# Performance work log

Hardware: AMD Instinct MI355X
Metric: run time of the kernel (lower is better)

The kernel has to match this reference:

```python
import jax, jax.numpy as jnp
from jax import lax
import numpy as np

TAG_NAMES = ["O", "B-MAT", "I-MAT", "B-PRO", "I-PRO", "B-APL", "I-APL", "B-SMT", "I-SMT", "B-CMT", "I-CMT", "B-DSC", "I-DSC"]
IMP = -100.0


def _init_crf_params(key):
    # torchcrf initializes uniform(-0.1, 0.1); CRF_NEW then clamps invalid
    # BIO transitions to -100 per define_invalid_crf_transitions/init_crf_transitions.
    K = len(TAG_NAMES)
    k1, k2, k3 = jax.random.split(key, 3)
    start = np.array(jax.random.uniform(k1, (K,), minval=-0.1, maxval=0.1), dtype=np.float32)
    end = np.array(jax.random.uniform(k2, (K,), minval=-0.1, maxval=0.1), dtype=np.float32)
    trans = np.array(jax.random.uniform(k3, (K, K), minval=-0.1, maxval=0.1), dtype=np.float32)
    pref = [t[0] for t in TAG_NAMES]
    ent = [t.split('-')[1] if '-' in t else '' for t in TAG_NAMES]
    for i in range(K):
        if pref[i] in ('B', 'I'):  # invalid begin/end for BIO
            start[i] = IMP
            end[i] = IMP
    for i in range(K):
        for j in range(K):
            # invalid_transitions_position: O -> I  (B->P, I->P are empty sets)
            if pref[i] == 'O' and pref[j] == 'I':
                trans[i, j] = IMP
            # invalid_transitions_tags: B->I, I->I across different entity types
            if pref[i] in ('B', 'I') and pref[j] == 'I' and ent[i] != ent[j]:
                trans[i, j] = IMP
    return jnp.asarray(start), jnp.asarray(end), jnp.asarray(trans)


def setup_inputs() -> dict:
    key = jax.random.key(0)
    k_em, k_tag, k_p = jax.random.split(key, 3)
    B, T, K = 4096, 512, len(TAG_NAMES)
    emissions = jax.random.normal(k_em, (B, T, K), dtype=jnp.float32)
    tags = jax.random.randint(k_tag, (B, T), 0, K, dtype=jnp.int64)
    mask = jnp.ones((B, T), dtype=bool)
    start_transitions, end_transitions, transitions = _init_crf_params(k_p)
    return {"emissions": emissions, "tags": tags, "mask": mask,
            "start_transitions": start_transitions,
            "end_transitions": end_transitions,
            "transitions": transitions}


def reference(emissions, tags, mask, start_transitions, end_transitions, transitions):
    # torchcrf CRF.forward with batch_first=True, reduction='sum':
    # returns sum over batch of log p(tags | emissions).
    B, T, K = emissions.shape
    maskf = mask.astype(emissions.dtype)

    # ---- numerator: score of the given tag path ----
    emit = jnp.take_along_axis(emissions, tags[..., None], axis=2)[..., 0]  # [B,T]
    trans = transitions[tags[:, :-1], tags[:, 1:]]                           # [B,T-1]
    num = start_transitions[tags[:, 0]] + emit[:, 0]
    num = num + jnp.sum((trans + emit[:, 1:]) * maskf[:, 1:], axis=1)
    seq_ends = jnp.sum(mask.astype(jnp.int32), axis=1) - 1                   # [B]
    last_tags = tags[jnp.arange(B), seq_ends]
    num = num + end_transitions[last_tags]

    # ---- denominator: log partition via forward-algorithm scan over time ----
    em_t = jnp.swapaxes(emissions, 0, 1)   # [T,B,K]
    mask_t = jnp.swapaxes(mask, 0, 1)      # [T,B]
    score0 = start_transitions + em_t[0]   # [B,K]

    def step(score, xs):
        em, m = xs  # em: [B,K], m: [B]
        # broadcast: [B,K_from,1] + [K_from,K_to] + [B,1,K_to]
        nxt = jax.nn.logsumexp(score[:, :, None] + transitions[None] + em[:, None, :], axis=1)
        return jnp.where(m[:, None], nxt, score), None

    score, _ = lax.scan(step, score0, (em_t[1:], mask_t[1:]))
    denom = jax.nn.logsumexp(score + end_transitions, axis=1)  # [B]

    return jnp.sum(num - denom)
```

## Files before the change

### kernel.cpp

```cpp
#include <hip/hip_runtime.h>


typedef float  f4  __attribute__((ext_vector_type(4)));
typedef float  f4u __attribute__((ext_vector_type(4), aligned(4)));
typedef int    i2  __attribute__((ext_vector_type(2)));
typedef int    i4  __attribute__((ext_vector_type(4)));
typedef __bf16 bh8 __attribute__((ext_vector_type(8)));

#define FENCE do { __builtin_amdgcn_sched_barrier(0); \
                   asm volatile("" ::: "memory"); } while (0)

__device__ __forceinline__ unsigned pack_bf16(float x, float y) {
  return __builtin_amdgcn_perm(__float_as_uint(y) + 0x8000u,
                               __float_as_uint(x) + 0x8000u, 0x07060302u);
}

__global__ void __launch_bounds__(128, 1)
crf_main(const float* __restrict__ em,
         const int*   __restrict__ tags,
         const float* __restrict__ startT,
         const float* __restrict__ endT,
         const float* __restrict__ trans,
         float* __restrict__ partial)
{
  __shared__ float ldsT[256];
  __shared__ float ldsS[16], ldsE[16];
  __shared__ float pFa[256];
  __shared__ float lsF[16], numF[16], resB[16];
  __shared__ int   tag255[16];

  const int tid = threadIdx.x;
  for (int i = tid; i < 169; i += 128) {
    const int r_ = i / 13, c_ = i - r_ * 13;
    ldsT[r_ * 16 + c_] = trans[i];
  }
  if (tid < 13) ldsS[tid] = startT[tid];
  if (tid >= 16 && tid < 29) ldsE[tid - 16] = endT[tid - 16];
  __syncthreads();

  const int lane = tid & 63;
  const int n    = lane & 15;
  const int q    = lane >> 4;
  const bool is_fwd = (tid < 64);
  const int seq  = blockIdx.x * 16 + n;
  const int loadBase = (q < 3) ? 4 * q : 9;
  const int lo       = (q < 3) ? 4 * q : 12;
  const unsigned span = (q < 3) ? 3u : 0u;
  const float* emP = em + (size_t)seq * 6656 + loadBase;
  const int*   tgP = tags + (size_t)seq * 512;

  bh8 afrag;
  {
    float av[4];
#pragma unroll
    for (int i = 0; i < 4; ++i) {
      const int kk = 4 * q + i;
      av[i] = (kk < 13 && n < 13)
            ? __expf(is_fwd ? ldsT[kk * 16 + n] : ldsT[n * 16 + kk]) : 0.0f;
    }
    i4 ai = { (int)pack_bf16(av[0], av[1]), (int)pack_bf16(av[2], av[3]), 0, 0 };
    afrag = __builtin_bit_cast(bh8, ai);
  }

  f4 D;
#pragma unroll
  for (int r = 0; r < 4; ++r) {
    const int m = 4 * q + r;
    D[r] = (m < 13) ? __expf(is_fwd ? ldsS[m] : ldsE[m]) : 0.0f;
  }

  int   ls2 = 0;
  int   epend = 0;
  float rcCur = 1.0f;
  float em_acc = 0.0f, trans_acc = 0.0f;
  float sDs0 = 0, sDs1 = 0, sDs2 = 0, sDs3 = 0;
  float start_t0 = 0.0f;
  int tg_hi = 0, tg_lo = 0, tg511 = 0;
  f4 eA[16], eB[16];
  int4 tA[4], tB[4];

#define TGV(TB, k) ((((k) & 3) == 0) ? TB[(k) >> 2].x : (((k) & 3) == 1) ? TB[(k) >> 2].y \
                  : (((k) & 3) == 2) ? TB[(k) >> 2].z : TB[(k) >> 2].w)

#define LOADC(EB, TB, TC) do {                                          \
    const int tc_ = (TC);                                               \
    _Pragma("unroll")                                                   \
    for (int k_ = 0; k_ < 16; ++k_)                                     \
      EB[k_] = *(const f4u*)(emP + (size_t)(tc_ + k_) * 13);            \
    _Pragma("unroll")                                                   \
    for (int g_ = 0; g_ < 4; ++g_)                                      \
      TB[g_] = *(const int4*)(tgP + tc_ + 4 * g_);                      \
  } while (0)

#define RNMEAS() do {                                                   \
    float cm_ = fmaxf(fmaxf(Ds0, Ds1), fmaxf(Ds2, Ds3));                \
    cm_ = fmaxf(cm_, __shfl_xor(cm_, 16, 64));                          \
    cm_ = fmaxf(cm_, __shfl_xor(cm_, 32, 64));                          \
    const int eb_ = (int)(__float_as_uint(cm_) >> 23);                  \
    epend = eb_ - 126;                                                  \
    rcCur = __uint_as_float((unsigned)(253 - eb_) << 23);               \
  } while (0)

#define CORE(EM4, KPH, TGVv) do {                                       \
    float e0 = __expf((q == 3) ? (EM4).w : (EM4).x);                    \
    float e1 = __expf((EM4).y);                                         \
    float e2 = __expf((EM4).z);                                         \
    float e3 = __expf((EM4).w);                                         \
    if ((KPH) == 7) { e0 *= rcCur; e1 *= rcCur; e2 *= rcCur; e3 *= rcCur; \
                      ls2 += epend; }                                   \
    Ds0 = D[0] * e0; Ds1 = D[1] * e1; Ds2 = D[2] * e2; Ds3 = D[3] * e3; \
    if ((KPH) == 5) RNMEAS();                                           \
    {                                                                   \
      const unsigned ur_ = (unsigned)((TGVv) - lo);                     \
      const int rr_ = (TGVv) - loadBase;                                \
      const float s01_ = (rr_ & 1) ? (EM4).y : (EM4).x;                 \
      const float s23_ = (rr_ & 1) ? (EM4).w : (EM4).z;                 \
      const float sv_  = (rr_ & 2) ? s23_ : s01_;                       \
      em_acc += (ur_ <= span) ? sv_ : 0.0f;                             \
    }                                                                   \
    {                                                                   \
      i4 bi_ = { (int)pack_bf16(Ds0, Ds1), (int)pack_bf16(Ds2, Ds3), 0, 0 }; \
      bh8 bf_ = __builtin_bit_cast(bh8, bi_);                           \
      D = __builtin_amdgcn_mfma_f32_16x16x32_bf16(                      \
              afrag, bf_, (f4){0.f, 0.f, 0.f, 0.f}, 0, 0, 0);           \
    }                                                                   \
  } while (0)

#define PROCF(EB, TB, FIRST, LAST) do {                                 \
    _Pragma("unroll")                                                   \
    for (int k = 0; k < 16; ++k) {                                      \
      const int tgv = TGV(TB, k);                                       \
      if (FIRST && k == 0) start_t0 = ldsS[tgv];                        \
      else {                                                            \
        const int pv = (k == 0) ? tg_hi : TGV(TB, k - 1);               \
        trans_acc += ldsT[pv * 16 + tgv];                               \
      }                                                                 \
      const f4 em4 = EB[k];                                             \
      float Ds0, Ds1, Ds2, Ds3;                                         \
      CORE(em4, (k & 7), tgv);                                          \
      if (LAST && k == 15) { sDs0 = Ds0; sDs1 = Ds1; sDs2 = Ds2; sDs3 = Ds3; } \
    }                                                                   \
    tg_hi = TGV(TB, 15);                                                \
  } while (0)

#define PROCB(EB, TB, FIRST) do {                                       \
    if (FIRST) tg511 = TGV(TB, 15);                                     \
    else       trans_acc += ldsT[TGV(TB, 15) * 16 + tg_lo];             \
    _Pragma("unroll")                                                   \
    for (int kk = 0; kk < 16; ++kk) {                                   \
      const int k = 15 - kk;                                            \
      const int tgv = TGV(TB, k);                                       \
      if (k > 0) trans_acc += ldsT[TGV(TB, k - 1) * 16 + tgv];          \
      const f4 em4 = EB[k];                                             \
      float Ds0, Ds1, Ds2, Ds3;                                         \
      CORE(em4, (kk & 7), tgv);                                         \
    }                                                                   \
    tg_lo = TGV(TB, 0);                                                 \
  } while (0)

  if (is_fwd) {
    LOADC(eA, tA, 0); LOADC(eB, tB, 16); FENCE;
    PROCF(eA, tA, true, false);
    for (int it = 0; it < 7; ++it) {
      LOADC(eA, tA, 32 * it + 32); FENCE;
      PROCF(eB, tB, false, false);
      LOADC(eB, tB, 32 * it + 48); FENCE;
      PROCF(eA, tA, false, false);
    }
    FENCE;
    PROCF(eB, tB, false, true);
    float emr = em_acc + __shfl_xor(em_acc, 16, 64);
    emr += __shfl_xor(emr, 32, 64);
    if (q == 0) {
      lsF[n]    = (float)ls2 * 0.6931471805599453f;
      numF[n]   = start_t0 + emr + trans_acc;
      tag255[n] = tg_hi;
    }
    *(f4*)&pFa[n * 16 + 4 * q] = (f4){sDs0, sDs1, sDs2, sDs3};
  } else {
    LOADC(eA, tA, 496); LOADC(eB, tB, 480); FENCE;
    PROCB(eA, tA, true);
    for (int it = 0; it < 7; ++it) {
      LOADC(eA, tA, 464 - 32 * it); FENCE;
      PROCB(eB, tB, false);
      LOADC(eB, tB, 448 - 32 * it); FENCE;
      PROCB(eA, tA, false);
    }
    FENCE;
    PROCB(eB, tB, false);
  }

  __syncthreads();

  if (!is_fwd) {
    const f4 al = *(const f4*)&pFa[n * 16 + 4 * q];
    float z = al[0] * D[0] + al[1] * D[1] + al[2] * D[2] + al[3] * D[3];
    z += __shfl_xor(z, 16, 64);
    z += __shfl_xor(z, 32, 64);
    float emr = em_acc + __shfl_xor(em_acc, 16, 64);
    emr += __shfl_xor(emr, 32, 64);
    const float denom = lsF[n] + (float)ls2 * 0.6931471805599453f + __logf(z);
    const float num   = numF[n] + emr + trans_acc
                      + ldsT[tag255[n] * 16 + tg_lo]
                      + ldsE[tg511];
    if (q == 0) resB[n] = num - denom;
  }
  __syncthreads();
  if (tid == 0) {
    float s = 0.0f;
#pragma unroll
    for (int i = 0; i < 16; ++i) s += resB[i];
    partial[blockIdx.x] = s;
  }

#undef TGV
#undef LOADC
#undef RNMEAS
#undef CORE
#undef PROCF
#undef PROCB
}

__global__ void __launch_bounds__(256)
crf_reduce(const float* __restrict__ part, float* __restrict__ out, int n)
{
  float v = 0.0f;
  for (int i = threadIdx.x; i < n; i += 256) v += part[i];
#pragma unroll
  for (int off = 32; off > 0; off >>= 1) v += __shfl_down(v, off);
  __shared__ float w[4];
  if ((threadIdx.x & 63) == 0) w[threadIdx.x >> 6] = v;
  __syncthreads();
  if (threadIdx.x == 0) out[0] = (w[0] + w[1]) + (w[2] + w[3]);
}

extern "C" void kernel_launch(void* const* d_in, const int* in_sizes, int n_in,
                              void* d_out, int out_size, void* d_ws, size_t ws_size,
                              hipStream_t stream) {
  const float* em   = (const float*)d_in[0];
  const int*   tags = (const int*)d_in[1];
  const float* st   = (const float*)d_in[3];
  const float* en   = (const float*)d_in[4];
  const float* tr   = (const float*)d_in[5];
  float* part = (float*)d_ws;

  crf_main<<<256, 128, 0, stream>>>(em, tags, st, en, tr, part);
  crf_reduce<<<1, 256, 0, stream>>>(part, (float*)d_out, 256);
}
```

Measured before the change: 186.8 us.

## Offload CRF numerator scoring to a dedicated third wavefront per block

Adds a third wave per block that computes the gold-path numerator (emission gather plus start, transition and end scores), splitting each sequence into four time chunks across lane groups. The forward and backward recurrence waves no longer load tags or accumulate numerator terms, which shortens their serial MFMA critical path. In exchange the new wave issues scattered scalar emission gathers that compete for memory bandwidth, and the block grows to 192 threads.

```diff
diff --git a/kernel.cpp b/kernel.cpp
--- a/kernel.cpp
+++ b/kernel.cpp
@@ -3,7 +3,6 @@
 
 typedef float  f4  __attribute__((ext_vector_type(4)));
 typedef float  f4u __attribute__((ext_vector_type(4), aligned(4)));
-typedef int    i2  __attribute__((ext_vector_type(2)));
 typedef int    i4  __attribute__((ext_vector_type(4)));
 typedef __bf16 bh8 __attribute__((ext_vector_type(8)));
 
@@ -15,7 +14,7 @@
                                __float_as_uint(x) + 0x8000u, 0x07060302u);
 }
 
-__global__ void __launch_bounds__(128, 1)
+__global__ void __launch_bounds__(192, 1)
 crf_main(const float* __restrict__ em,
          const int*   __restrict__ tags,
          const float* __restrict__ startT,
@@ -27,10 +26,9 @@
   __shared__ float ldsS[16], ldsE[16];
   __shared__ float pFa[256];
   __shared__ float lsF[16], numF[16], resB[16];
-  __shared__ int   tag255[16];
 
   const int tid = threadIdx.x;
-  for (int i = tid; i < 169; i += 128) {
+  for (int i = tid; i < 169; i += 192) {
     const int r_ = i / 13, c_ = i - r_ * 13;
     ldsT[r_ * 16 + c_] = trans[i];
   }
@@ -39,57 +37,74 @@
   __syncthreads();
 
   const int lane = tid & 63;
+  const int wv   = tid >> 6;
   const int n    = lane & 15;
   const int q    = lane >> 4;
-  const bool is_fwd = (tid < 64);
-  const int seq  = blockIdx.x * 16 + n;
-  const int loadBase = (q < 3) ? 4 * q : 9;
-  const int lo       = (q < 3) ? 4 * q : 12;
-  const unsigned span = (q < 3) ? 3u : 0u;
-  const float* emP = em + (size_t)seq * 6656 + loadBase;
-  const int*   tgP = tags + (size_t)seq * 512;
-
-  bh8 afrag;
-  {
-    float av[4];
-#pragma unroll
-    for (int i = 0; i < 4; ++i) {
-      const int kk = 4 * q + i;
-      av[i] = (kk < 13 && n < 13)
-            ? __expf(is_fwd ? ldsT[kk * 16 + n] : ldsT[n * 16 + kk]) : 0.0f;
-    }
-    i4 ai = { (int)pack_bf16(av[0], av[1]), (int)pack_bf16(av[2], av[3]), 0, 0 };
-    afrag = __builtin_bit_cast(bh8, ai);
-  }
-
-  f4 D;
-#pragma unroll
-  for (int r = 0; r < 4; ++r) {
-    const int m = 4 * q + r;
-    D[r] = (m < 13) ? __expf(is_fwd ? ldsS[m] : ldsE[m]) : 0.0f;
-  }
-
-  int   ls2 = 0;
-  int   epend = 0;
-  float rcCur = 1.0f;
-  float em_acc = 0.0f, trans_acc = 0.0f;
+
+  f4  D = {0.f, 0.f, 0.f, 0.f};
+  int ls2 = 0;
   float sDs0 = 0, sDs1 = 0, sDs2 = 0, sDs3 = 0;
-  float start_t0 = 0.0f;
-  int tg_hi = 0, tg_lo = 0, tg511 = 0;
-  f4 eA[16], eB[16];
-  int4 tA[4], tB[4];
-
-#define TGV(TB, k) ((((k) & 3) == 0) ? TB[(k) >> 2].x : (((k) & 3) == 1) ? TB[(k) >> 2].y \
-                  : (((k) & 3) == 2) ? TB[(k) >> 2].z : TB[(k) >> 2].w)
-
-#define LOADC(EB, TB, TC) do {                                          \
+
+  if (wv == 2) {
+    const int s = q;
+    const int seq = blockIdx.x * 16 + n;
+    const int* tq = tags + (size_t)seq * 512;
+    const float* emQ = em + (size_t)seq * 6656;
+    const int t0base = 128 * s;
+    float nacc = 0.0f;
+    int prev = (s > 0) ? tq[t0base - 1] : 0;
+#pragma unroll 4
+    for (int g = 0; g < 32; ++g) {
+      const int t0 = t0base + 4 * g;
+      const int4 tv = *(const int4*)(tq + t0);
+      nacc += emQ[(size_t)(t0 + 0) * 13 + tv.x];
+      nacc += emQ[(size_t)(t0 + 1) * 13 + tv.y];
+      nacc += emQ[(size_t)(t0 + 2) * 13 + tv.z];
+      nacc += emQ[(size_t)(t0 + 3) * 13 + tv.w];
+      if (!(s == 0 && g == 0)) nacc += ldsT[prev * 16 + tv.x];
+      nacc += ldsT[tv.x * 16 + tv.y] + ldsT[tv.y * 16 + tv.z]
+            + ldsT[tv.z * 16 + tv.w];
+      prev = tv.w;
+    }
+    if (s == 0) nacc += ldsS[tq[0]];
+    if (s == 3) nacc += ldsE[prev];
+    nacc += __shfl_xor(nacc, 16, 64);
+    nacc += __shfl_xor(nacc, 32, 64);
+    if (s == 0) numF[n] = nacc;
+  } else {
+    const bool is_fwd = (wv == 0);
+    const int seq = blockIdx.x * 16 + n;
+    const int loadBase = (q < 3) ? 4 * q : 9;
+    const float* emP = em + (size_t)seq * 6656 + loadBase;
+
+    bh8 afrag;
+    {
+      float av[4];
+#pragma unroll
+      for (int i = 0; i < 4; ++i) {
+        const int kk = 4 * q + i;
+        av[i] = (kk < 13 && n < 13)
+              ? __expf(is_fwd ? ldsT[kk * 16 + n] : ldsT[n * 16 + kk]) : 0.0f;
+      }
+      i4 ai = { (int)pack_bf16(av[0], av[1]), (int)pack_bf16(av[2], av[3]), 0, 0 };
+      afrag = __builtin_bit_cast(bh8, ai);
+    }
+
+#pragma unroll
+    for (int r = 0; r < 4; ++r) {
+      const int m = 4 * q + r;
+      D[r] = (m < 13) ? __expf(is_fwd ? ldsS[m] : ldsE[m]) : 0.0f;
+    }
+
+    int   epend = 0;
+    float rcCur = 1.0f;
+    f4 eA[16], eB[16];
+
+#define LOADE(EB, TC) do {                                              \
     const int tc_ = (TC);                                               \
     _Pragma("unroll")                                                   \
     for (int k_ = 0; k_ < 16; ++k_)                                     \
       EB[k_] = *(const f4u*)(emP + (size_t)(tc_ + k_) * 13);            \
-    _Pragma("unroll")                                                   \
-    for (int g_ = 0; g_ < 4; ++g_)                                      \
-      TB[g_] = *(const int4*)(tgP + tc_ + 4 * g_);                      \
   } while (0)
 
 #define RNMEAS() do {                                                   \
@@ -101,7 +116,7 @@
     rcCur = __uint_as_float((unsigned)(253 - eb_) << 23);               \
   } while (0)
 
-#define CORE(EM4, KPH, TGVv) do {                                       \
+#define CORE(EM4, KPH) do {                                             \
     float e0 = __expf((q == 3) ? (EM4).w : (EM4).x);                    \
     float e1 = __expf((EM4).y);                                         \
     float e2 = __expf((EM4).z);                                         \
@@ -111,14 +126,6 @@
     Ds0 = D[0] * e0; Ds1 = D[1] * e1; Ds2 = D[2] * e2; Ds3 = D[3] * e3; \
     if ((KPH) == 5) RNMEAS();                                           \
     {                                                                   \
-      const unsigned ur_ = (unsigned)((TGVv) - lo);                     \
-      const int rr_ = (TGVv) - loadBase;                                \
-      const float s01_ = (rr_ & 1) ? (EM4).y : (EM4).x;                 \
-      const float s23_ = (rr_ & 1) ? (EM4).w : (EM4).z;                 \
-      const float sv_  = (rr_ & 2) ? s23_ : s01_;                       \
-      em_acc += (ur_ <= span) ? sv_ : 0.0f;                             \
-    }                                                                   \
-    {                                                                   \
       i4 bi_ = { (int)pack_bf16(Ds0, Ds1), (int)pack_bf16(Ds2, Ds3), 0, 0 }; \
       bh8 bf_ = __builtin_bit_cast(bh8, bi_);                           \
       D = __builtin_amdgcn_mfma_f32_16x16x32_bf16(                      \
@@ -126,84 +133,66 @@
     }                                                                   \
   } while (0)
 
-#define PROCF(EB, TB, FIRST, LAST) do {                                 \
+#define PROCF(EB, LAST) do {                                            \
     _Pragma("unroll")                                                   \
     for (int k = 0; k < 16; ++k) {                                      \
-      const int tgv = TGV(TB, k);                                       \
-      if (FIRST && k == 0) start_t0 = ldsS[tgv];                        \
-      else {                                                            \
-        const int pv = (k == 0) ? tg_hi : TGV(TB, k - 1);               \
-        trans_acc += ldsT[pv * 16 + tgv];                               \
-      }                                                                 \
       const f4 em4 = EB[k];                                             \
       float Ds0, Ds1, Ds2, Ds3;                                         \
-      CORE(em4, (k & 7), tgv);                                          \
-      if (LAST && k == 15) { sDs0 = Ds0; sDs1 = Ds1; sDs2 = Ds2; sDs3 = Ds3; } \
+      CORE(em4, (k & 7));                                               \
+      if ((LAST) && k == 15) { sDs0 = Ds0; sDs1 = Ds1; sDs2 = Ds2; sDs3 = Ds3; } \
     }                                                                   \
-    tg_hi = TGV(TB, 15);                                                \
-  } while (0)
-
-#define PROCB(EB, TB, FIRST) do {                                       \
-    if (FIRST) tg511 = TGV(TB, 15);                                     \
-    else       trans_acc += ldsT[TGV(TB, 15) * 16 + tg_lo];             \
+  } while (0)
+
+#define PROCB(EB) do {                                                  \
     _Pragma("unroll")                                                   \
     for (int kk = 0; kk < 16; ++kk) {                                   \
-      const int k = 15 - kk;                                            \
-      const int tgv = TGV(TB, k);                                       \
-      if (k > 0) trans_acc += ldsT[TGV(TB, k - 1) * 16 + tgv];          \
-      const f4 em4 = EB[k];                                             \
+      const f4 em4 = EB[15 - kk];                                       \
       float Ds0, Ds1, Ds2, Ds3;                                         \
-      CORE(em4, (kk & 7), tgv);                                         \
+      CORE(em4, (kk & 7));                                              \
     }                                                                   \
-    tg_lo = TGV(TB, 0);                                                 \
-  } while (0)
-
-  if (is_fwd) {
-    LOADC(eA, tA, 0); LOADC(eB, tB, 16); FENCE;
-    PROCF(eA, tA, true, false);
-    for (int it = 0; it < 7; ++it) {
-      LOADC(eA, tA, 32 * it + 32); FENCE;
-      PROCF(eB, tB, false, false);
-      LOADC(eB, tB, 32 * it + 48); FENCE;
-      PROCF(eA, tA, false, false);
-    }
-    FENCE;
-    PROCF(eB, tB, false, true);
-    float emr = em_acc + __shfl_xor(em_acc, 16, 64);
-    emr += __shfl_xor(emr, 32, 64);
-    if (q == 0) {
-      lsF[n]    = (float)ls2 * 0.6931471805599453f;
-      numF[n]   = start_t0 + emr + trans_acc;
-      tag255[n] = tg_hi;
-    }
-    *(f4*)&pFa[n * 16 + 4 * q] = (f4){sDs0, sDs1, sDs2, sDs3};
-  } else {
-    LOADC(eA, tA, 496); LOADC(eB, tB, 480); FENCE;
-    PROCB(eA, tA, true);
-    for (int it = 0; it < 7; ++it) {
-      LOADC(eA, tA, 464 - 32 * it); FENCE;
-      PROCB(eB, tB, false);
-      LOADC(eB, tB, 448 - 32 * it); FENCE;
-      PROCB(eA, tA, false);
-    }
-    FENCE;
-    PROCB(eB, tB, false);
-  }
-
-  __syncthreads();
-
-  if (!is_fwd) {
+  } while (0)
+
+    if (is_fwd) {
+      LOADE(eA, 0); LOADE(eB, 16); FENCE;
+      PROCF(eA, false);
+      for (int it = 0; it < 7; ++it) {
+        LOADE(eA, 32 * it + 32); FENCE;
+        PROCF(eB, false);
+        LOADE(eB, 32 * it + 48); FENCE;
+        PROCF(eA, false);
+      }
+      FENCE;
+      PROCF(eB, true);
+      if (q == 0) lsF[n] = (float)ls2 * 0.6931471805599453f;
+      *(f4*)&pFa[n * 16 + 4 * q] = (f4){sDs0, sDs1, sDs2, sDs3};
+    } else {
+      LOADE(eA, 496); LOADE(eB, 480); FENCE;
+      PROCB(eA);
+      for (int it = 0; it < 7; ++it) {
+        LOADE(eA, 464 - 32 * it); FENCE;
+        PROCB(eB);
+        LOADE(eB, 448 - 32 * it); FENCE;
+        PROCB(eA);
+      }
+      FENCE;
+      PROCB(eB);
+    }
+#undef LOADE
+#undef RNMEAS
+#undef CORE
+#undef PROCF
+#undef PROCB
+  }
+
+  __syncthreads();
+
+  if (wv == 1) {
     const f4 al = *(const f4*)&pFa[n * 16 + 4 * q];
     float z = al[0] * D[0] + al[1] * D[1] + al[2] * D[2] + al[3] * D[3];
     z += __shfl_xor(z, 16, 64);
     z += __shfl_xor(z, 32, 64);
-    float emr = em_acc + __shfl_xor(em_acc, 16, 64);
-    emr += __shfl_xor(emr, 32, 64);
     const float denom = lsF[n] + (float)ls2 * 0.6931471805599453f + __logf(z);
-    const float num   = numF[n] + emr + trans_acc
-                      + ldsT[tag255[n] * 16 + tg_lo]
-                      + ldsE[tg511];
-    if (q == 0) resB[n] = num - denom;
+    if (q == 0) resB[n] = numF[n] - denom;
   }
   __syncthreads();
   if (tid == 0) {
@@ -212,13 +201,6 @@
     for (int i = 0; i < 16; ++i) s += resB[i];
     partial[blockIdx.x] = s;
   }
-
-#undef TGV
-#undef LOADC
-#undef RNMEAS
-#undef CORE
-#undef PROCF
-#undef PROCB
 }
 
 __global__ void __launch_bounds__(256)
@@ -244,6 +226,6 @@
   const float* tr   = (const float*)d_in[5];
   float* part = (float*)d_ws;
 
-  crf_main<<<256, 128, 0, stream>>>(em, tags, st, en, tr, part);
+  crf_main<<<256, 192, 0, stream>>>(em, tags, st, en, tr, part);
   crf_reduce<<<1, 256, 0, stream>>>(part, (float*)d_out, 256);
 }
```

Result: slower. 190.8 us (+2.1%).
